# Kernel tuning notes

Hardware: AMD Instinct MI355X
Metric: run time of the kernel (lower is better)

The kernel has to match this reference:

```python
import jax, jax.numpy as jnp
import numpy as np

HIDDEN = 1024
HEADS = 16
HEAD = HIDDEN // HEADS  # 64, rotary_emb_dim == head dim
B = 8
S = 1024  # max_seqlen; all sequences full length
WINDOW = (64, 64)  # sliding_window=128 -> (64, 64)
ROPE_BASE = 10000.0


def _rope_cos_sin(seqlen, dim, base):
    inv_freq = 1.0 / (base ** (jnp.arange(0, dim, 2, dtype=jnp.float32) / dim))
    t = jnp.arange(seqlen, dtype=jnp.float32)
    freqs = jnp.outer(t, inv_freq)  # [S, dim/2]
    return jnp.cos(freqs), jnp.sin(freqs)


def _apply_rope(x, cos, sin):
    # x: [B, S, H, D], non-interleaved rotary over full head dim
    d2 = cos.shape[-1]
    x1, x2 = x[..., :d2], x[..., d2:]
    c = cos[None, :, None, :]
    s = sin[None, :, None, :]
    return jnp.concatenate([x1 * c - x2 * s, x2 * c + x1 * s], axis=-1)


def setup_inputs() -> dict:
    key = jax.random.key(0)
    k1, k2, k3 = jax.random.split(key, 3)
    hidden_states = jax.random.normal(k1, (B * S, HIDDEN), dtype=jnp.float32)
    cu_seqlens = jnp.arange(B + 1, dtype=jnp.int32) * S
    indices = jnp.arange(B * S, dtype=jnp.int32)
    attn_mask = jnp.ones((B, S), dtype=jnp.int32)
    Wqkv = jax.random.normal(k2, (3 * HIDDEN, HIDDEN), dtype=jnp.float32) * 0.02
    Wo = jax.random.normal(k3, (HIDDEN, HIDDEN), dtype=jnp.float32) * 0.02
    return {
        'hidden_states': hidden_states,
        'cu_seqlens': cu_seqlens,
        'max_seqlen': S,
        'indices': indices,
        'attn_mask': attn_mask,
        'Wqkv': Wqkv,
        'Wo': Wo,
    }


def reference(hidden_states, cu_seqlens, max_seqlen, indices, attn_mask, Wqkv, Wo):
    # QKV projection on unpadded tokens: [T, 3*H*D]
    qkv = hidden_states @ Wqkv.T
    qkv = qkv.reshape(B, S, 3, HEADS, HEAD)
    # Rotary positions reset per sequence; all sequences are full length S.
    cos, sin = _rope_cos_sin(S, HEAD, ROPE_BASE)
    q = _apply_rope(qkv[:, :, 0], cos, sin)
    k = _apply_rope(qkv[:, :, 1], cos, sin)
    v = qkv[:, :, 2]
    scores = jnp.einsum('bshd,bthd->bhst', q, k) / jnp.sqrt(jnp.float32(HEAD))
    # sliding-window mask: key j visible to query i iff i-left <= j <= i+right
    i = jnp.arange(S)[:, None]
    j = jnp.arange(S)[None, :]
    win = (j >= i - WINDOW[0]) & (j <= i + WINDOW[1])  # [S, S]
    key_mask = attn_mask.astype(bool)[:, None, None, :]  # [B,1,1,S]
    mask = win[None, None, :, :] & key_mask
    scores = jnp.where(mask, scores, jnp.finfo(scores.dtype).min)
    probs = jax.nn.softmax(scores, axis=-1)
    attn = jnp.einsum('bhst,bthd->bshd', probs, v).reshape(B * S, HIDDEN)
    return attn @ Wo.T
```

## Files before the change

### kernel.cpp

```cpp
#include <hip/hip_runtime.h>


typedef __attribute__((ext_vector_type(8))) short short8;
typedef __attribute__((ext_vector_type(4))) float f32x4;

#define SEQ   1024
#define NHEAD 16
#define HEADD 64
#define NTOK  8192

__device__ __forceinline__ unsigned short f2bf(float x) {
  unsigned u = __float_as_uint(x);
  u += 0x7fffu + ((u >> 16) & 1u);
  return (unsigned short)(u >> 16);
}

__device__ __forceinline__ void gload_lds16(const void* g, void* l) {
  __builtin_amdgcn_global_load_lds((__attribute__((address_space(1))) void*)(g),
                                   (__attribute__((address_space(3))) void*)(l),
                                   16, 0, 0);
}

__global__ __launch_bounds__(256) void prep(
    const float* __restrict__ hidden, const float* __restrict__ Wqkv,
    const float* __restrict__ Wo,
    unsigned short* __restrict__ hb, unsigned short* __restrict__ wqb,
    unsigned short* __restrict__ wob, float2* __restrict__ tab) {
  int bid = blockIdx.x;
  const float* in; unsigned short* out; int i;
  if (bid < 8192)       { in = hidden; out = hb;  i = bid * 256 + threadIdx.x; }
  else if (bid < 11264) { in = Wqkv;   out = wqb; i = (bid - 8192) * 256 + threadIdx.x; }
  else if (bid < 12288) { in = Wo;     out = wob; i = (bid - 11264) * 256 + threadIdx.x; }
  else {
    int j = (bid - 12288) * 256 + threadIdx.x;
    int s = j >> 5, d = j & 31;
    float inv = exp2f(-(float)d * 0.41524101186092034f);
    float sn, cs;
    sincosf((float)s * inv, &sn, &cs);
    tab[j] = make_float2(cs, sn);
    return;
  }
  float4 v = ((const float4*)in)[i];
  ushort4 o;
  o.x = f2bf(v.x); o.y = f2bf(v.y); o.z = f2bf(v.z); o.w = f2bf(v.w);
  ((ushort4*)out)[i] = o;
}

__global__ __launch_bounds__(256) void gemm_qkv_rope(
    const unsigned short* __restrict__ A,
    const unsigned short* __restrict__ W,
    const float2* __restrict__ tab,
    unsigned short* __restrict__ qb,
    unsigned short* __restrict__ kb,
    unsigned short* __restrict__ vt)
{
  __shared__ unsigned short As[2][128 * 64];
  __shared__ unsigned short Bs[2][128 * 64];
  const int tid  = threadIdx.x;
  const int wave = tid >> 6, lane = tid & 63;
  const int quad = lane >> 4, l15 = lane & 15;
  const int bid  = blockIdx.x;
  const int xcd  = bid & 7, idx = bid >> 3;
  const int rb   = xcd * 8 + (idx & 7);
  const int cb   = idx >> 3;
  const int row0 = rb * 128;
  const int col0 = cb * 128;
  const int mrow = (wave >> 1) * 64;
  const int ncol = (wave & 1) * 64;
  const int l7x8 = (l15 & 7) * 8;

  f32x4 acc[4][4];
#pragma unroll
  for (int i = 0; i < 4; i++)
#pragma unroll
    for (int j = 0; j < 4; j++) acc[i][j] = (f32x4){0.f, 0.f, 0.f, 0.f};

  auto stage = [&](int bi, int k0) {
#pragma unroll
    for (int i = 0; i < 4; i++) {
      int p = i * 256 + tid;
      int r = p >> 3, c = p & 7;
      int cs = c ^ (r & 7);
      gload_lds16(A + (size_t)(row0 + r) * 1024 + k0 + cs * 8, &As[bi][p * 8]);
      gload_lds16(W + (size_t)(col0 + r) * 1024 + k0 + cs * 8, &Bs[bi][p * 8]);
    }
  };

  stage(0, 0);
  __syncthreads();
  int buf = 0;
  for (int k0 = 0; k0 < 1024; k0 += 64) {
    if (k0 + 64 < 1024) stage(buf ^ 1, k0 + 64);
#pragma unroll
    for (int kk = 0; kk < 2; kk++) {
      const int qs8 = ((kk * 4 + quad) * 8) ^ l7x8;
      short8 af[4], bfr[4];
#pragma unroll
      for (int mt = 0; mt < 4; mt++)
        af[mt] = *(const short8*)&As[buf][(mrow + mt * 16 + l15) * 64 + qs8];
#pragma unroll
      for (int nt = 0; nt < 4; nt++)
        bfr[nt] = *(const short8*)&Bs[buf][(ncol + nt * 16 + l15) * 64 + qs8];
#pragma unroll
      for (int mt = 0; mt < 4; mt++)
#pragma unroll
        for (int nt = 0; nt < 4; nt++)
          acc[mt][nt] = __builtin_amdgcn_mfma_f32_16x16x32_bf16(af[mt], bfr[nt],
                                                                acc[mt][nt], 0, 0, 0);
    }
    __syncthreads();
    buf ^= 1;
  }

  const int colw  = col0 + ncol;
  const int which = colw >> 10;
  const int h     = (colw >> 6) & 15;
  const int rowg  = row0 + mrow;

  if (which == 2) {
#pragma unroll
    for (int mt = 0; mt < 4; mt++) {
      int rbase = rowg + mt * 16 + quad * 4;
      int b = rbase >> 10, s = rbase & 1023;
#pragma unroll
      for (int c = 0; c < 4; c++) {
        int d = c * 16 + l15;
        ushort4 o;
        o.x = f2bf(acc[mt][c][0]); o.y = f2bf(acc[mt][c][1]);
        o.z = f2bf(acc[mt][c][2]); o.w = f2bf(acc[mt][c][3]);
        *(ushort4*)&vt[((size_t)((b * 16 + h) * 64 + d)) * 1024 + s] = o;
      }
    }
  } else {
    unsigned short* dst = (which == 0) ? qb : kb;
    const float scale = (which == 0) ? 0.125f : 1.0f;
#pragma unroll
    for (int mt = 0; mt < 4; mt++) {
#pragma unroll
      for (int r = 0; r < 4; r++) {
        int row = rowg + mt * 16 + quad * 4 + r;
        int b = row >> 10, s = row & 1023;
        size_t base = (size_t)((b * 16 + h) * 1024 + s) * 64;
        float2 t0 = tab[s * 32 + l15];
        float2 t1 = tab[s * 32 + 16 + l15];
        float x1a = acc[mt][0][r], x2a = acc[mt][2][r];
        float x1b = acc[mt][1][r], x2b = acc[mt][3][r];
        dst[base + l15]           = f2bf((x1a * t0.x - x2a * t0.y) * scale);
        dst[base + 32 + l15]      = f2bf((x2a * t0.x + x1a * t0.y) * scale);
        dst[base + 16 + l15]      = f2bf((x1b * t1.x - x2b * t1.y) * scale);
        dst[base + 48 + l15]      = f2bf((x2b * t1.x + x1b * t1.y) * scale);
      }
    }
  }
}

__global__ __launch_bounds__(512) void attn_win(
    const unsigned short* __restrict__ qb,
    const unsigned short* __restrict__ kb,
    const unsigned short* __restrict__ vt,
    const int* __restrict__ am,
    unsigned short* __restrict__ ob)
{
  __shared__ unsigned short KP[20992];
  __shared__ unsigned short Vs[64 * 260];
  __shared__ unsigned short smask[256];

  const int tid  = threadIdx.x;
  const int wave = tid >> 6, lane = tid & 63;
  const int quad = lane >> 4, l15 = lane & 15;
  const int b  = blockIdx.x >> 4, h = blockIdx.x & 15;
  const int qs = blockIdx.y * 128;
  const size_t hb = (size_t)(b * 16 + h);
  const unsigned short* Qg = qb + hb * SEQ * 64;
  const unsigned short* Kg = kb + hb * SEQ * 64;
  const unsigned short* Vg = vt + hb * 64 * SEQ;
  const int t0 = qs - 64;

#pragma unroll
  for (int i = 0; i < 4; i++) {
    int p = i * 512 + tid;
    int r = p >> 3, c = p & 7;
    int t = t0 + r; t = t < 0 ? 0 : (t > 1023 ? 1023 : t);
    *(short8*)&KP[r * 68 + c * 8] = *(const short8*)&Kg[(size_t)t * 64 + c * 8];
  }
  short8 vreg[4]; int vdst[4];
#pragma unroll
  for (int i = 0; i < 4; i++) {
    int p = i * 512 + tid;
    int d = p >> 5, c = p & 31;
    int t = t0 + c * 8; t = t < 0 ? 0 : (t > 1016 ? 1016 : t);
    vreg[i] = *(const short8*)&Vg[(size_t)d * SEQ + t];
    vdst[i] = d * 260 + c * 8;
  }
  if (tid < 64) {
    Vs[tid * 260 + 256] = 0; Vs[tid * 260 + 257] = 0;
    Vs[tid * 260 + 258] = 0; Vs[tid * 260 + 259] = 0;
  }
  if (tid < 256) {
    int t = t0 + tid;
    smask[tid] = (t >= 0 && t < SEQ) ? (unsigned short)(am[b * SEQ + t] != 0) : 0;
  }
  __syncthreads();

  const int qw = qs + wave * 16;
  short8 qf0 = *(const short8*)&Qg[(size_t)(qw + l15) * 64 + quad * 8];
  short8 qf1 = *(const short8*)&Qg[(size_t)(qw + l15) * 64 + 32 + quad * 8];

  f32x4 sc[9];
#pragma unroll
  for (int tt2 = 0; tt2 < 9; tt2++) {
    int kr = (wave + tt2) * 16 + l15;
    short8 b0 = *(const short8*)&KP[kr * 68 + quad * 8];
    short8 b1 = *(const short8*)&KP[kr * 68 + 32 + quad * 8];
    f32x4 a = (f32x4){0.f, 0.f, 0.f, 0.f};
    a = __builtin_amdgcn_mfma_f32_16x16x32_bf16(qf0, b0, a, 0, 0, 0);
    a = __builtin_amdgcn_mfma_f32_16x16x32_bf16(qf1, b1, a, 0, 0, 0);
    sc[tt2] = a;
  }

  float lrow[4];
#pragma unroll
  for (int r = 0; r < 4; r++) {
    int i = qw + quad * 4 + r;
    float sum = 0.f;
#pragma unroll
    for (int tt2 = 0; tt2 < 9; tt2++) {
      int kl = (wave + tt2) * 16 + l15;
      int t = t0 + kl;
      bool ok = (t >= i - 64) && (t <= i + 64) && smask[kl];
      float p = ok ? __expf(sc[tt2][r]) : 0.f;
      sc[tt2][r] = p;
      sum += p;
    }
#pragma unroll
    for (int off = 1; off < 16; off <<= 1) sum += __shfl_xor(sum, off);
    lrow[r] = sum;
  }

  __syncthreads();
#pragma unroll
  for (int i = 0; i < 4; i++)
    *(short8*)&Vs[vdst[i]] = vreg[i];
  unsigned short* Pw = &KP[wave * (16 * 164)];
#pragma unroll
  for (int tt2 = 0; tt2 < 9; tt2++)
#pragma unroll
    for (int r = 0; r < 4; r++)
      Pw[(quad * 4 + r) * 164 + tt2 * 16 + l15] = f2bf(sc[tt2][r]);
#pragma unroll
  for (int r = 0; r < 4; r++)
    Pw[(quad * 4 + r) * 164 + 144 + l15] = 0;
  __syncthreads();

  f32x4 o[4];
#pragma unroll
  for (int dt = 0; dt < 4; dt++) o[dt] = (f32x4){0.f, 0.f, 0.f, 0.f};
#pragma unroll
  for (int kt = 0; kt < 5; kt++) {
    short8 pf = *(const short8*)&Pw[l15 * 164 + kt * 32 + quad * 8];
#pragma unroll
    for (int dt = 0; dt < 4; dt++) {
      short8 vf = *(const short8*)&Vs[(dt * 16 + l15) * 260 +
                                      wave * 16 + kt * 32 + quad * 8];
      o[dt] = __builtin_amdgcn_mfma_f32_16x16x32_bf16(pf, vf, o[dt], 0, 0, 0);
    }
  }

#pragma unroll
  for (int r = 0; r < 4; r++) {
    float inv = 1.f / lrow[r];
    int tok = b * SEQ + qw + quad * 4 + r;
    size_t base = (size_t)tok * 1024 + h * 64;
#pragma unroll
    for (int dt = 0; dt < 4; dt++)
      ob[base + dt * 16 + l15] = f2bf(o[dt][r] * inv);
  }
}

__global__ __launch_bounds__(256) void gemm_out(
    const unsigned short* __restrict__ A,
    const unsigned short* __restrict__ W,
    float* __restrict__ out)
{
  __shared__ unsigned short As[2][128 * 64];
  __shared__ unsigned short Bs[2][128 * 64];
  const int tid  = threadIdx.x;
  const int wave = tid >> 6, lane = tid & 63;
  const int quad = lane >> 4, l15 = lane & 15;
  const int bid  = blockIdx.x;
  const int xcd  = bid & 7, idx = bid >> 3;
  const int row0 = (xcd * 8 + (idx & 7)) * 128;
  const int col0 = (idx >> 3) * 128;
  const int mrow = (wave >> 1) * 64;
  const int ncol = (wave & 1) * 64;
  const int l7x8 = (l15 & 7) * 8;

  f32x4 acc[4][4];
#pragma unroll
  for (int i = 0; i < 4; i++)
#pragma unroll
    for (int j = 0; j < 4; j++) acc[i][j] = (f32x4){0.f, 0.f, 0.f, 0.f};

  auto stage = [&](int bi, int k0) {
#pragma unroll
    for (int i = 0; i < 4; i++) {
      int p = i * 256 + tid;
      int r = p >> 3, c = p & 7;
      int cs = c ^ (r & 7);
      gload_lds16(A + (size_t)(row0 + r) * 1024 + k0 + cs * 8, &As[bi][p * 8]);
      gload_lds16(W + (size_t)(col0 + r) * 1024 + k0 + cs * 8, &Bs[bi][p * 8]);
    }
  };

  stage(0, 0);
  __syncthreads();
  int buf = 0;
  for (int k0 = 0; k0 < 1024; k0 += 64) {
    if (k0 + 64 < 1024) stage(buf ^ 1, k0 + 64);
#pragma unroll
    for (int kk = 0; kk < 2; kk++) {
      const int qs8 = ((kk * 4 + quad) * 8) ^ l7x8;
      short8 af[4], bfr[4];
#pragma unroll
      for (int mt = 0; mt < 4; mt++)
        af[mt] = *(const short8*)&As[buf][(mrow + mt * 16 + l15) * 64 + qs8];
#pragma unroll
      for (int nt = 0; nt < 4; nt++)
        bfr[nt] = *(const short8*)&Bs[buf][(ncol + nt * 16 + l15) * 64 + qs8];
#pragma unroll
      for (int mt = 0; mt < 4; mt++)
#pragma unroll
        for (int nt = 0; nt < 4; nt++)
          acc[mt][nt] = __builtin_amdgcn_mfma_f32_16x16x32_bf16(af[mt], bfr[nt],
                                                                acc[mt][nt], 0, 0, 0);
    }
    __syncthreads();
    buf ^= 1;
  }

  const int colw = col0 + ncol;
  const int rowg = row0 + mrow;
#pragma unroll
  for (int mt = 0; mt < 4; mt++)
#pragma unroll
    for (int r = 0; r < 4; r++) {
      int row = rowg + mt * 16 + quad * 4 + r;
#pragma unroll
      for (int nt = 0; nt < 4; nt++)
        out[(size_t)row * 1024 + colw + nt * 16 + l15] = acc[mt][nt][r];
    }
}

extern "C" void kernel_launch(void* const* d_in, const int* in_sizes, int n_in,
                              void* d_out, int out_size, void* d_ws, size_t ws_size,
                              hipStream_t stream) {
  const float* hidden = (const float*)d_in[0];
  const int*   am     = (const int*)d_in[4];
  const float* Wqkv   = (const float*)d_in[5];
  const float* Wo     = (const float*)d_in[6];
  float* out = (float*)d_out;

  char* ws = (char*)d_ws;
  unsigned short* hb  = (unsigned short*)(ws);
  unsigned short* wqb = (unsigned short*)(ws + (size_t)(16 << 20));
  unsigned short* wob = (unsigned short*)(ws + (size_t)(22 << 20));
  unsigned short* qbf = (unsigned short*)(ws + (size_t)(24 << 20));
  unsigned short* kbf = (unsigned short*)(ws + (size_t)(40 << 20));
  unsigned short* vtb = (unsigned short*)(ws + (size_t)(56 << 20));
  float2*         tab = (float2*)(ws + (size_t)(72 << 20));
  unsigned short* ab  = hb;

  prep<<<12416, 256, 0, stream>>>(hidden, Wqkv, Wo, hb, wqb, wob, tab);

  gemm_qkv_rope<<<1536, 256, 0, stream>>>(hb, wqb, tab, qbf, kbf, vtb);

  dim3 g2(128, 8);
  attn_win<<<g2, 512, 0, stream>>>(qbf, kbf, vtb, am, ab);

  gemm_out<<<512, 256, 0, stream>>>(ab, wob, out);
}
```

Measured before the change: 208.7 us.

## Enlarge QKV GEMM tile to 256x256 with 8 waves and split A/B staging

The QKV projection GEMM moves from 128x128 tiles with 4 waves to 256x256 tiles with 8 waves. Each wave now computes 128x64 in two halves, and loads of A and B are staged separately behind explicit vmcnt waits and raw barriers. The aim is to raise arithmetic intensity per LDS byte and overlap global loads with MFMA work, with s_setprio raising priority during the MFMA bursts. In exchange the LDS footprint grows to 128KB per block, the grid shrinks to 384 blocks so occupancy drops, and the block-to-XCD mapping changes.

```diff
diff --git a/kernel.cpp b/kernel.cpp
--- a/kernel.cpp
+++ b/kernel.cpp
@@ -46,7 +46,7 @@
   ((ushort4*)out)[i] = o;
 }
 
-__global__ __launch_bounds__(256) void gemm_qkv_rope(
+__global__ __launch_bounds__(512) void gemm_qkv_rope(
     const unsigned short* __restrict__ A,
     const unsigned short* __restrict__ W,
     const float2* __restrict__ tab,
@@ -54,62 +54,112 @@
     unsigned short* __restrict__ kb,
     unsigned short* __restrict__ vt)
 {
-  __shared__ unsigned short As[2][128 * 64];
-  __shared__ unsigned short Bs[2][128 * 64];
+  __shared__ unsigned short As[2][256 * 64];
+  __shared__ unsigned short Bs[2][256 * 64];
   const int tid  = threadIdx.x;
   const int wave = tid >> 6, lane = tid & 63;
   const int quad = lane >> 4, l15 = lane & 15;
+  const int wm   = wave >> 2, wn = wave & 3;
   const int bid  = blockIdx.x;
-  const int xcd  = bid & 7, idx = bid >> 3;
-  const int rb   = xcd * 8 + (idx & 7);
-  const int cb   = idx >> 3;
-  const int row0 = rb * 128;
-  const int col0 = cb * 128;
-  const int mrow = (wave >> 1) * 64;
-  const int ncol = (wave & 1) * 64;
+  const int wg   = (bid & 7) * 48 + (bid >> 3);
+  const int rb   = wg & 31, cb = wg >> 5;
+  const int row0 = rb * 256;
+  const int col0 = cb * 256;
+  const int mrow = wm * 128;
+  const int ncol = wn * 64;
   const int l7x8 = (l15 & 7) * 8;
 
-  f32x4 acc[4][4];
-#pragma unroll
-  for (int i = 0; i < 4; i++)
+  const unsigned short* gA[4]; const unsigned short* gB[4]; int lofs[4];
+#pragma unroll
+  for (int j = 0; j < 4; ++j) {
+    int p = j * 512 + tid;
+    int r = p >> 3, c = p & 7;
+    int cs = c ^ (r & 7);
+    gA[j]  = A + (size_t)(row0 + r) * 1024 + cs * 8;
+    gB[j]  = W + (size_t)(col0 + r) * 1024 + cs * 8;
+    lofs[j] = p * 8;
+  }
+  auto stageA = [&](int bi, int k0) {
+#pragma unroll
+    for (int j = 0; j < 4; ++j) gload_lds16(gA[j] + k0, &As[bi][lofs[j]]);
+  };
+  auto stageB = [&](int bi, int k0) {
+#pragma unroll
+    for (int j = 0; j < 4; ++j) gload_lds16(gB[j] + k0, &Bs[bi][lofs[j]]);
+  };
+
+  f32x4 acc[8][4];
+#pragma unroll
+  for (int i = 0; i < 8; i++)
 #pragma unroll
     for (int j = 0; j < 4; j++) acc[i][j] = (f32x4){0.f, 0.f, 0.f, 0.f};
 
-  auto stage = [&](int bi, int k0) {
-#pragma unroll
-    for (int i = 0; i < 4; i++) {
-      int p = i * 256 + tid;
-      int r = p >> 3, c = p & 7;
-      int cs = c ^ (r & 7);
-      gload_lds16(A + (size_t)(row0 + r) * 1024 + k0 + cs * 8, &As[bi][p * 8]);
-      gload_lds16(W + (size_t)(col0 + r) * 1024 + k0 + cs * 8, &Bs[bi][p * 8]);
-    }
-  };
-
-  stage(0, 0);
-  __syncthreads();
-  int buf = 0;
-  for (int k0 = 0; k0 < 1024; k0 += 64) {
-    if (k0 + 64 < 1024) stage(buf ^ 1, k0 + 64);
-#pragma unroll
-    for (int kk = 0; kk < 2; kk++) {
-      const int qs8 = ((kk * 4 + quad) * 8) ^ l7x8;
-      short8 af[4], bfr[4];
+  stageA(0, 0); stageB(0, 0);
+
+#pragma unroll 1
+  for (int t = 0; t < 16; ++t) {
+    const int bi = t & 1;
+    if (t < 15) {
+      stageA(bi ^ 1, (t + 1) * 64);
+      asm volatile("s_waitcnt vmcnt(4)" ::: "memory");
+    } else {
+      asm volatile("s_waitcnt vmcnt(0)" ::: "memory");
+    }
+    __builtin_amdgcn_s_barrier();
+    {
+      short8 af[4][2], bf[4][2];
 #pragma unroll
       for (int mt = 0; mt < 4; mt++)
-        af[mt] = *(const short8*)&As[buf][(mrow + mt * 16 + l15) * 64 + qs8];
+#pragma unroll
+        for (int kk = 0; kk < 2; kk++)
+          af[mt][kk] = *(const short8*)&As[bi][(mrow + mt * 16 + l15) * 64 +
+                                              (((kk * 4 + quad) * 8) ^ l7x8)];
 #pragma unroll
       for (int nt = 0; nt < 4; nt++)
-        bfr[nt] = *(const short8*)&Bs[buf][(ncol + nt * 16 + l15) * 64 + qs8];
+#pragma unroll
+        for (int kk = 0; kk < 2; kk++)
+          bf[nt][kk] = *(const short8*)&Bs[bi][(ncol + nt * 16 + l15) * 64 +
+                                              (((kk * 4 + quad) * 8) ^ l7x8)];
+      __builtin_amdgcn_s_setprio(1);
+#pragma unroll
+      for (int kk = 0; kk < 2; kk++)
+#pragma unroll
+        for (int mt = 0; mt < 4; mt++)
+#pragma unroll
+          for (int nt = 0; nt < 4; nt++)
+            acc[mt][nt] = __builtin_amdgcn_mfma_f32_16x16x32_bf16(
+                af[mt][kk], bf[nt][kk], acc[mt][nt], 0, 0, 0);
+      __builtin_amdgcn_s_setprio(0);
+    }
+    __builtin_amdgcn_s_barrier();
+    if (t < 15) stageB(bi ^ 1, (t + 1) * 64);
+    __builtin_amdgcn_s_barrier();
+    {
+      short8 af[4][2], bf[4][2];
 #pragma unroll
       for (int mt = 0; mt < 4; mt++)
 #pragma unroll
-        for (int nt = 0; nt < 4; nt++)
-          acc[mt][nt] = __builtin_amdgcn_mfma_f32_16x16x32_bf16(af[mt], bfr[nt],
-                                                                acc[mt][nt], 0, 0, 0);
-    }
-    __syncthreads();
-    buf ^= 1;
+        for (int kk = 0; kk < 2; kk++)
+          af[mt][kk] = *(const short8*)&As[bi][(mrow + 64 + mt * 16 + l15) * 64 +
+                                              (((kk * 4 + quad) * 8) ^ l7x8)];
+#pragma unroll
+      for (int nt = 0; nt < 4; nt++)
+#pragma unroll
+        for (int kk = 0; kk < 2; kk++)
+          bf[nt][kk] = *(const short8*)&Bs[bi][(ncol + nt * 16 + l15) * 64 +
+                                              (((kk * 4 + quad) * 8) ^ l7x8)];
+      __builtin_amdgcn_s_setprio(1);
+#pragma unroll
+      for (int kk = 0; kk < 2; kk++)
+#pragma unroll
+        for (int mt = 0; mt < 4; mt++)
+#pragma unroll
+          for (int nt = 0; nt < 4; nt++)
+            acc[4 + mt][nt] = __builtin_amdgcn_mfma_f32_16x16x32_bf16(
+                af[mt][kk], bf[nt][kk], acc[4 + mt][nt], 0, 0, 0);
+      __builtin_amdgcn_s_setprio(0);
+    }
+    __builtin_amdgcn_s_barrier();
   }
 
   const int colw  = col0 + ncol;
@@ -119,8 +169,9 @@
 
   if (which == 2) {
 #pragma unroll
-    for (int mt = 0; mt < 4; mt++) {
-      int rbase = rowg + mt * 16 + quad * 4;
+    for (int mt = 0; mt < 8; mt++) {
+      int rowOff = (mt >> 2) * 64 + (mt & 3) * 16;
+      int rbase = rowg + rowOff + quad * 4;
       int b = rbase >> 10, s = rbase & 1023;
 #pragma unroll
       for (int c = 0; c < 4; c++) {
@@ -135,10 +186,11 @@
     unsigned short* dst = (which == 0) ? qb : kb;
     const float scale = (which == 0) ? 0.125f : 1.0f;
 #pragma unroll
-    for (int mt = 0; mt < 4; mt++) {
+    for (int mt = 0; mt < 8; mt++) {
+      int rowOff = (mt >> 2) * 64 + (mt & 3) * 16;
 #pragma unroll
       for (int r = 0; r < 4; r++) {
-        int row = rowg + mt * 16 + quad * 4 + r;
+        int row = rowg + rowOff + quad * 4 + r;
         int b = row >> 10, s = row & 1023;
         size_t base = (size_t)((b * 16 + h) * 1024 + s) * 64;
         float2 t0 = tab[s * 32 + l15];
@@ -372,7 +424,7 @@
 
   prep<<<12416, 256, 0, stream>>>(hidden, Wqkv, Wo, hb, wqb, wob, tab);
 
-  gemm_qkv_rope<<<1536, 256, 0, stream>>>(hb, wqb, tab, qbf, kbf, vtb);
+  gemm_qkv_rope<<<384, 512, 0, stream>>>(hb, wqb, tab, qbf, kbf, vtb);
 
   dim3 g2(128, 8);
   attn_win<<<g2, 512, 0, stream>>>(qbf, kbf, vtb, am, ab);
```

Result: slower. 240.1 us (+15.0%).

## Compute transposed scores so P stays in registers for PV MFMA

Applied to the files above, without the earlier changes.

Swaps the QK^T MFMA operands so each lane holds a column of keys for one query. The bf16 probabilities can then feed a 16x16x16 MFMA directly as the B operand, with no round trip through LDS and no extra barrier. The output is written as packed 4-element stores. The row-sum reduction shrinks to two shuffles. In exchange, the PV step uses twice as many smaller MFMAs (9 k-steps of 16) over per-wave V reads.

```diff
diff --git a/kernel.cpp b/kernel.cpp
--- a/kernel.cpp
+++ b/kernel.cpp
@@ -2,6 +2,7 @@
 
 
 typedef __attribute__((ext_vector_type(8))) short short8;
+typedef __attribute__((ext_vector_type(4))) short short4v;
 typedef __attribute__((ext_vector_type(4))) float f32x4;
 
 #define SEQ   1024
@@ -14,6 +15,17 @@
   u += 0x7fffu + ((u >> 16) & 1u);
   return (unsigned short)(u >> 16);
 }
+
+#if __has_builtin(__builtin_amdgcn_mfma_f32_16x16x16bf16_1k)
+__device__ __forceinline__ f32x4 mfma16(short4v a, short4v b, f32x4 c) {
+  return __builtin_amdgcn_mfma_f32_16x16x16bf16_1k(a, b, c, 0, 0, 0);
+}
+#else
+__device__ __forceinline__ f32x4 mfma16(short4v a, short4v b, f32x4 c) {
+  asm("v_mfma_f32_16x16x16_bf16 %0, %1, %2, %0" : "+v"(c) : "v"(a), "v"(b));
+  return c;
+}
+#endif
 
 __device__ __forceinline__ void gload_lds16(const void* g, void* l) {
   __builtin_amdgcn_global_load_lds((__attribute__((address_space(1))) void*)(g),
@@ -161,7 +173,7 @@
     const int* __restrict__ am,
     unsigned short* __restrict__ ob)
 {
-  __shared__ unsigned short KP[20992];
+  __shared__ unsigned short Ks[256 * 68];
   __shared__ unsigned short Vs[64 * 260];
   __shared__ unsigned short smask[256];
 
@@ -181,7 +193,7 @@
     int p = i * 512 + tid;
     int r = p >> 3, c = p & 7;
     int t = t0 + r; t = t < 0 ? 0 : (t > 1023 ? 1023 : t);
-    *(short8*)&KP[r * 68 + c * 8] = *(const short8*)&Kg[(size_t)t * 64 + c * 8];
+    *(short8*)&Ks[r * 68 + c * 8] = *(const short8*)&Kg[(size_t)t * 64 + c * 8];
   }
   short8 vreg[4]; int vdst[4];
 #pragma unroll
@@ -192,10 +204,6 @@
     vreg[i] = *(const short8*)&Vg[(size_t)d * SEQ + t];
     vdst[i] = d * 260 + c * 8;
   }
-  if (tid < 64) {
-    Vs[tid * 260 + 256] = 0; Vs[tid * 260 + 257] = 0;
-    Vs[tid * 260 + 258] = 0; Vs[tid * 260 + 259] = 0;
-  }
   if (tid < 256) {
     int t = t0 + tid;
     smask[tid] = (t >= 0 && t < SEQ) ? (unsigned short)(am[b * SEQ + t] != 0) : 0;
@@ -210,70 +218,65 @@
 #pragma unroll
   for (int tt2 = 0; tt2 < 9; tt2++) {
     int kr = (wave + tt2) * 16 + l15;
-    short8 b0 = *(const short8*)&KP[kr * 68 + quad * 8];
-    short8 b1 = *(const short8*)&KP[kr * 68 + 32 + quad * 8];
+    short8 a0 = *(const short8*)&Ks[kr * 68 + quad * 8];
+    short8 a1 = *(const short8*)&Ks[kr * 68 + 32 + quad * 8];
     f32x4 a = (f32x4){0.f, 0.f, 0.f, 0.f};
-    a = __builtin_amdgcn_mfma_f32_16x16x32_bf16(qf0, b0, a, 0, 0, 0);
-    a = __builtin_amdgcn_mfma_f32_16x16x32_bf16(qf1, b1, a, 0, 0, 0);
+    a = __builtin_amdgcn_mfma_f32_16x16x32_bf16(a0, qf0, a, 0, 0, 0);
+    a = __builtin_amdgcn_mfma_f32_16x16x32_bf16(a1, qf1, a, 0, 0, 0);
     sc[tt2] = a;
   }
 
-  float lrow[4];
-#pragma unroll
-  for (int r = 0; r < 4; r++) {
-    int i = qw + quad * 4 + r;
-    float sum = 0.f;
-#pragma unroll
-    for (int tt2 = 0; tt2 < 9; tt2++) {
-      int kl = (wave + tt2) * 16 + l15;
+  const int iq = qw + l15;
+  float sum = 0.f;
+#pragma unroll
+  for (int tt2 = 0; tt2 < 9; tt2++)
+#pragma unroll
+    for (int r = 0; r < 4; r++) {
+      int kl = (wave + tt2) * 16 + quad * 4 + r;
       int t = t0 + kl;
-      bool ok = (t >= i - 64) && (t <= i + 64) && smask[kl];
+      bool ok = (t >= iq - 64) && (t <= iq + 64) && smask[kl];
       float p = ok ? __expf(sc[tt2][r]) : 0.f;
       sc[tt2][r] = p;
       sum += p;
     }
-#pragma unroll
-    for (int off = 1; off < 16; off <<= 1) sum += __shfl_xor(sum, off);
-    lrow[r] = sum;
-  }
-
-  __syncthreads();
+  sum += __shfl_xor(sum, 16);
+  sum += __shfl_xor(sum, 32);
+
+  short4v pb[9];
+#pragma unroll
+  for (int tt2 = 0; tt2 < 9; tt2++) {
+    short4v pv;
+    pv[0] = (short)f2bf(sc[tt2][0]); pv[1] = (short)f2bf(sc[tt2][1]);
+    pv[2] = (short)f2bf(sc[tt2][2]); pv[3] = (short)f2bf(sc[tt2][3]);
+    pb[tt2] = pv;
+  }
+
 #pragma unroll
   for (int i = 0; i < 4; i++)
     *(short8*)&Vs[vdst[i]] = vreg[i];
-  unsigned short* Pw = &KP[wave * (16 * 164)];
-#pragma unroll
-  for (int tt2 = 0; tt2 < 9; tt2++)
-#pragma unroll
-    for (int r = 0; r < 4; r++)
-      Pw[(quad * 4 + r) * 164 + tt2 * 16 + l15] = f2bf(sc[tt2][r]);
-#pragma unroll
-  for (int r = 0; r < 4; r++)
-    Pw[(quad * 4 + r) * 164 + 144 + l15] = 0;
   __syncthreads();
 
   f32x4 o[4];
 #pragma unroll
   for (int dt = 0; dt < 4; dt++) o[dt] = (f32x4){0.f, 0.f, 0.f, 0.f};
 #pragma unroll
-  for (int kt = 0; kt < 5; kt++) {
-    short8 pf = *(const short8*)&Pw[l15 * 164 + kt * 32 + quad * 8];
+  for (int tt2 = 0; tt2 < 9; tt2++) {
+    int vcol = (wave + tt2) * 16 + quad * 4;
 #pragma unroll
     for (int dt = 0; dt < 4; dt++) {
-      short8 vf = *(const short8*)&Vs[(dt * 16 + l15) * 260 +
-                                      wave * 16 + kt * 32 + quad * 8];
-      o[dt] = __builtin_amdgcn_mfma_f32_16x16x32_bf16(pf, vf, o[dt], 0, 0, 0);
-    }
-  }
-
-#pragma unroll
-  for (int r = 0; r < 4; r++) {
-    float inv = 1.f / lrow[r];
-    int tok = b * SEQ + qw + quad * 4 + r;
-    size_t base = (size_t)tok * 1024 + h * 64;
-#pragma unroll
-    for (int dt = 0; dt < 4; dt++)
-      ob[base + dt * 16 + l15] = f2bf(o[dt][r] * inv);
+      short4v vf = *(const short4v*)&Vs[(dt * 16 + l15) * 260 + vcol];
+      o[dt] = mfma16(vf, pb[tt2], o[dt]);
+    }
+  }
+
+  const float inv = 1.f / sum;
+  const size_t base = (size_t)(b * SEQ + qw + l15) * 1024 + h * 64;
+#pragma unroll
+  for (int dt = 0; dt < 4; dt++) {
+    ushort4 ov;
+    ov.x = f2bf(o[dt][0] * inv); ov.y = f2bf(o[dt][1] * inv);
+    ov.z = f2bf(o[dt][2] * inv); ov.w = f2bf(o[dt][3] * inv);
+    *(ushort4*)&ob[base + dt * 16 + quad * 4] = ov;
   }
 }
 
```

Result: no change. 211.8 us (+1.5%).
